# Kernel tuning notes

Measured on AMD Instinct MI355X. Metric: run time of the kernel, lower is better.

## Reference

```python
import jax, jax.numpy as jnp
import numpy as np

B, H, W, C = 64, 56, 56, 192
NH, WS, SS = 6, 7, 3          # heads, window size, shift size
N = WS * WS                   # tokens per window = 49
NW = (H // WS) * (W // WS)    # windows per image = 64
HD = C // NH                  # head dim = 32
SCALE = HD ** -0.5
EPS = 1e-5


def _rel_pos_index():
    coords = np.stack(np.meshgrid(np.arange(WS), np.arange(WS), indexing='ij'))  # [2,WS,WS]
    flat = coords.reshape(2, -1)                                                  # [2,N]
    rel = (flat[:, :, None] - flat[:, None, :]).transpose(1, 2, 0)                # [N,N,2]
    rel[..., 0] += WS - 1
    rel[..., 1] += WS - 1
    rel[..., 0] *= 2 * WS - 1
    return jnp.asarray(rel.sum(-1))  # [N,N] int

REL_IDX = _rel_pos_index()


def _shift_mask():
    # standard Swin shifted-window attention mask: 0 within region, -100 across
    img = np.zeros((H, W), dtype=np.float32)
    cnt = 0
    for hs in (slice(0, -WS), slice(-WS, -SS), slice(-SS, None)):
        for ws in (slice(0, -WS), slice(-WS, -SS), slice(-SS, None)):
            img[hs, ws] = cnt
            cnt += 1
    win = img.reshape(H // WS, WS, W // WS, WS).transpose(0, 2, 1, 3).reshape(NW, N)
    diff = win[:, None, :] - win[:, :, None]
    return jnp.asarray(np.where(diff != 0, -100.0, 0.0).astype(np.float32))  # [NW,N,N]


def setup_inputs() -> dict:
    key = jax.random.key(0)
    ks = jax.random.split(key, 8)
    s = 0.02
    return {
        'x': jax.random.normal(ks[0], (B, H, W, C), jnp.float32),
        'mask_matrix': _shift_mask(),
        'norm1_g': jnp.ones((C,), jnp.float32),
        'norm1_b': jnp.zeros((C,), jnp.float32),
        'qkv_w': jax.random.normal(ks[1], (3 * C, C), jnp.float32) * s,
        'qkv_b': jnp.zeros((3 * C,), jnp.float32),
        'rpb_table': jax.random.normal(ks[2], ((2 * WS - 1) ** 2, NH), jnp.float32) * s,
        'proj_w': jax.random.normal(ks[3], (C, C), jnp.float32) * s,
        'proj_b': jnp.zeros((C,), jnp.float32),
        'norm2_g': jnp.ones((C,), jnp.float32),
        'norm2_b': jnp.zeros((C,), jnp.float32),
        'fc1_w': jax.random.normal(ks[4], (4 * C, C), jnp.float32) * s,
        'fc1_b': jnp.zeros((4 * C,), jnp.float32),
        'fc2_w': jax.random.normal(ks[5], (C, 4 * C), jnp.float32) * s,
        'fc2_b': jnp.zeros((C,), jnp.float32),
    }


def _ln(x, g, b):
    m = jnp.mean(x, axis=-1, keepdims=True)
    v = jnp.mean(jnp.square(x - m), axis=-1, keepdims=True)
    return (x - m) * jax.lax.rsqrt(v + EPS) * g + b


def _block(x, mask_matrix, norm1_g, norm1_b, qkv_w, qkv_b, rpb_table,
           proj_w, proj_b, norm2_g, norm2_b, fc1_w, fc1_b, fc2_w, fc2_b):
    shortcut = x
    xn = _ln(x, norm1_g, norm1_b)
    # cyclic shift
    xs = jnp.roll(xn, (-SS, -SS), axis=(1, 2))
    # window partition -> [B*NW, N, C]
    win = xs.reshape(B, H // WS, WS, W // WS, WS, C).transpose(0, 1, 3, 2, 4, 5).reshape(B * NW, N, C)
    # qkv projection
    qkv = jnp.einsum('wnc,dc->wnd', win, qkv_w) + qkv_b           # [B*NW, N, 3C]
    qkv = qkv.reshape(B * NW, N, 3, NH, HD).transpose(2, 0, 3, 1, 4)
    q, k, v = qkv[0], qkv[1], qkv[2]                               # [B*NW, NH, N, HD]
    attn = jnp.einsum('whqd,whkd->whqk', q * SCALE, k)             # [B*NW, NH, N, N]
    # relative position bias gather
    bias = rpb_table[REL_IDX.reshape(-1)].reshape(N, N, NH).transpose(2, 0, 1)  # [NH,N,N]
    attn = attn + bias[None]
    # shifted-window mask
    attn = attn.reshape(B, NW, NH, N, N) + mask_matrix[None, :, None]
    attn = jax.nn.softmax(attn.reshape(B * NW, NH, N, N), axis=-1)
    out = jnp.einsum('whqk,whkd->whqd', attn, v)                   # [B*NW, NH, N, HD]
    out = out.transpose(0, 2, 1, 3).reshape(B * NW, N, C)
    out = jnp.einsum('wnc,dc->wnd', out, proj_w) + proj_b
    # window reverse + reverse shift
    xr = out.reshape(B, H // WS, W // WS, WS, WS, C).transpose(0, 1, 3, 2, 4, 5).reshape(B, H, W, C)
    xr = jnp.roll(xr, (SS, SS), axis=(1, 2))
    x = shortcut + xr
    # MLP
    xn2 = _ln(x, norm2_g, norm2_b)
    h = jax.nn.gelu(jnp.einsum('bhwc,dc->bhwd', xn2, fc1_w) + fc1_b, approximate=False)
    x = x + jnp.einsum('bhwd,cd->bhwc', h, fc2_w) + fc2_b
    return x


def reference(x, mask_matrix, norm1_g, norm1_b, qkv_w, qkv_b, rpb_table,
              proj_w, proj_b, norm2_g, norm2_b, fc1_w, fc1_b, fc2_w, fc2_b):
    return _block(x, mask_matrix, norm1_g, norm1_b, qkv_w, qkv_b, rpb_table,
                  proj_w, proj_b, norm2_g, norm2_b, fc1_w, fc1_b, fc2_w, fc2_b)
```

## Files before the change

kernel.cpp:

```cpp
#include <hip/hip_runtime.h>
#include <hip/hip_bf16.h>
#include <math.h>

typedef __attribute__((ext_vector_type(8))) short s16x8;
typedef __attribute__((ext_vector_type(4))) float f32x4;

static constexpr float cSCALE = 0.17677669529663687f;

__device__ __forceinline__ float bf2f(unsigned short u) {
    union { unsigned int i; float f; } c; c.i = ((unsigned int)u) << 16; return c.f;
}
__device__ __forceinline__ unsigned short f2bf(float f) {
    union { float f; unsigned int i; } c; c.f = f;
    unsigned int r = c.i + (0x7fffu + ((c.i >> 16) & 1u));
    return (unsigned short)(r >> 16);
}
__device__ __forceinline__ s16x8 cvt8(const float4 a, const float4 b) {
    s16x8 r;
    r[0]=(short)f2bf(a.x); r[1]=(short)f2bf(a.y); r[2]=(short)f2bf(a.z); r[3]=(short)f2bf(a.w);
    r[4]=(short)f2bf(b.x); r[5]=(short)f2bf(b.y); r[6]=(short)f2bf(b.z); r[7]=(short)f2bf(b.w);
    return r;
}
__device__ __forceinline__ float gelu_f(float t) {
    const float u = 1.5957691216057308f * t * (1.0f + 0.044715f * t * t);
    return t / (1.0f + __expf(-u));
}

#define GLDS16(gp, lp) __builtin_amdgcn_global_load_lds( \
    (const __attribute__((address_space(1))) void*)(gp), \
    (__attribute__((address_space(3))) void*)(lp), 16, 0, 0)

__device__ __forceinline__ void ln_frag(const float* __restrict__ rowp,
                                        const float* __restrict__ g,
                                        const float* __restrict__ b,
                                        int hi, s16x8* xa)
{
    float4 v[12];
    #pragma unroll
    for (int k = 0; k < 6; ++k) {
        v[2*k]   = *(const float4*)(rowp + k*32 + hi*8);
        v[2*k+1] = *(const float4*)(rowp + k*32 + hi*8 + 4);
    }
    float sm = 0.f, sq = 0.f;
    #pragma unroll
    for (int i = 0; i < 12; ++i) {
        sm += (v[i].x + v[i].y) + (v[i].z + v[i].w);
        sq += (v[i].x*v[i].x + v[i].y*v[i].y) + (v[i].z*v[i].z + v[i].w*v[i].w);
    }
    sm += __shfl_xor(sm, 16); sq += __shfl_xor(sq, 16);
    sm += __shfl_xor(sm, 32); sq += __shfl_xor(sq, 32);
    const float mean = sm * (1.0f/192.0f);
    const float rstd = rsqrtf(sq * (1.0f/192.0f) - mean*mean + 1e-5f);
    #pragma unroll
    for (int k = 0; k < 6; ++k) {
        const float4 ga = *(const float4*)(g + k*32 + hi*8);
        const float4 gb = *(const float4*)(g + k*32 + hi*8 + 4);
        const float4 ba = *(const float4*)(b + k*32 + hi*8);
        const float4 bb = *(const float4*)(b + k*32 + hi*8 + 4);
        s16x8 r;
        r[0] = (short)f2bf((v[2*k].x  -mean)*rstd*ga.x + ba.x);
        r[1] = (short)f2bf((v[2*k].y  -mean)*rstd*ga.y + ba.y);
        r[2] = (short)f2bf((v[2*k].z  -mean)*rstd*ga.z + ba.z);
        r[3] = (short)f2bf((v[2*k].w  -mean)*rstd*ga.w + ba.w);
        r[4] = (short)f2bf((v[2*k+1].x-mean)*rstd*gb.x + bb.x);
        r[5] = (short)f2bf((v[2*k+1].y-mean)*rstd*gb.y + bb.y);
        r[6] = (short)f2bf((v[2*k+1].z-mean)*rstd*gb.z + bb.z);
        r[7] = (short)f2bf((v[2*k+1].w-mean)*rstd*gb.w + bb.w);
        xa[k] = r;
    }
}

__global__ __launch_bounds__(256)
void pack_w(const float* __restrict__ qkvw, const float* __restrict__ pw,
            const float* __restrict__ f1w, const float* __restrict__ f2w,
            unsigned short* __restrict__ o)
{
    const int t = blockIdx.x * 256 + threadIdx.x;
    const int lane = t & 63, f = t >> 6;
    const int ln = lane & 15, ko = (lane >> 4) * 8;
    const float* src;
    if (f < 216) {
        const int h = f / 36, r = f - h * 36, nf = r / 6, kf = r - nf * 6;
        src = qkvw + (size_t)((nf >> 1) * 192 + h * 32 + (nf & 1) * 16 + ln) * 192 + kf * 32 + ko;
    } else if (f < 288) {
        const int g = f - 216, h = g / 12, nf = g - h * 12;
        src = pw + (size_t)(nf * 16 + ln) * 192 + h * 32 + ko;
    } else {
        const int g = f - 288;
        const int c = g / 24, r24 = g - c * 24;
        if (r24 < 12) {
            const int nf = r24 / 6, kf = r24 - nf * 6;
            src = f1w + (size_t)(c * 32 + nf * 16 + ln) * 192 + kf * 32 + ko;
        } else {
            const int nf = r24 - 12;
            src = f2w + (size_t)(nf * 16 + ln) * 768 + c * 32 + ko;
        }
    }
    *(s16x8*)(o + (size_t)t * 8) = cvt8(*(const float4*)src, *(const float4*)(src + 4));
}

__global__ __launch_bounds__(256)
void pack_bias(const float* __restrict__ mask, const float* __restrict__ rpb,
               unsigned short* __restrict__ o)
{
    const int wi = blockIdx.x / 6, h = blockIdx.x - wi * 6;
    for (int t = threadIdx.x; t < 49 * 64; t += 256) {
        const int n = t >> 6, mm = t & 63;
        const int ln = mm >> 2, nf = mm & 3;
        const int m = nf * 16 + ln;
        float v = 0.f;
        if (m < 49) {
            const int p1 = n / 7, q1 = n - p1 * 7, p2 = m / 7, q2 = m - p2 * 7;
            const int ridx = (p1 - p2 + 6) * 13 + (q1 - q2 + 6);
            v = rpb[ridx * 6 + h] + mask[(size_t)wi * 2401 + n * 49 + m];
        }
        o[(size_t)(wi * 6 + h) * 49 * 64 + t] = f2bf(v);
    }
}

__global__ __launch_bounds__(256, 4)
void swin_attn(const float* __restrict__ x, const float* __restrict__ g1,
               const float* __restrict__ b1, const unsigned short* __restrict__ wp,
               const unsigned short* __restrict__ bias_g,
               const float* __restrict__ qkvb, const float* __restrict__ pb,
               float* __restrict__ y)
{
    __shared__ __align__(16) unsigned short q_[64][40];
    __shared__ __align__(16) unsigned short o_[64][40];
    __shared__ __align__(16) unsigned short k2_[2][64][40];
    __shared__ __align__(16) unsigned short vt2_[2][32][72];
    __shared__ __align__(16) unsigned short p_[64][72];

    const s16x8* wv = (const s16x8*)wp;
    const int w  = blockIdx.x;
    const int bb = w >> 6, wi = w & 63;
    const int wh = wi >> 3, ww = wi & 7;
    const int tid = threadIdx.x, lane = tid & 63, wave = tid >> 6;
    const int ln = lane & 15, hi = lane >> 4, ko = hi * 8, ro = hi * 4;
    const int m0 = wave * 16;

    s16x8 xa[6];
    {
        const int t = m0 + ln;
        const int p = t / 7, q7 = t - p * 7;
        int i2 = wh * 7 + p + 3;  if (i2 >= 56) i2 -= 56;
        int j2 = ww * 7 + q7 + 3; if (j2 >= 56) j2 -= 56;
        const float* xr = x + ((size_t)(bb * 56 + i2) * 56 + j2) * 192;
        ln_frag(xr, g1, b1, hi, xa);
        if (t >= 49) {
            #pragma unroll
            for (int k = 0; k < 6; ++k) xa[k] = s16x8{0,0,0,0,0,0,0,0};
        }
    }

    auto qkv_head = [&](int hh) {
        const s16x8* wq = wv + ((size_t)(hh * 36) << 6);
        #pragma unroll
        for (int nf = 0; nf < 6; ++nf) {
            s16x8 bf6[6];
            #pragma unroll
            for (int kf = 0; kf < 6; ++kf) bf6[kf] = wq[(nf * 6 + kf) * 64 + lane];
            f32x4 a = f32x4{0.f,0.f,0.f,0.f};
            #pragma unroll
            for (int kf = 0; kf < 6; ++kf)
                a = __builtin_amdgcn_mfma_f32_16x16x32_bf16(xa[kf], bf6[kf], a, 0, 0, 0);
            const int col = nf * 16 + ln;
            #pragma unroll
            for (int i = 0; i < 4; ++i) {
                const int row = m0 + ro + i;
                const float v = a[i];
                if (nf < 2)      q_[row][col]                 = f2bf((v + qkvb[hh*32 + col]) * cSCALE);
                else if (nf < 4) k2_[hh & 1][row][col - 32]   = f2bf(v + qkvb[192 + hh*32 + col - 32]);
                else             vt2_[hh & 1][col - 64][row]  = f2bf(v + qkvb[384 + hh*32 + col - 64]);
            }
        }
    };

    qkv_head(0);

    f32x4 accp[12];
    #pragma unroll
    for (int i = 0; i < 12; ++i) accp[i] = f32x4{0.f,0.f,0.f,0.f};

    for (int h = 0; h < 6; ++h) {
        __syncthreads();

        f32x4 s4[4];
        {
            const s16x8 aq = *(const s16x8*)&q_[m0 + ln][ko];
            #pragma unroll
            for (int nf = 0; nf < 4; ++nf) {
                const s16x8 bk = *(const s16x8*)&k2_[h & 1][nf * 16 + ln][ko];
                s4[nf] = __builtin_amdgcn_mfma_f32_16x16x32_bf16(aq, bk, f32x4{0.f,0.f,0.f,0.f}, 0, 0, 0);
            }
        }
        const unsigned short* bg = bias_g + (size_t)(wi * 6 + h) * 49 * 64;
        float inv4[4];
        #pragma unroll
        for (int i = 0; i < 4; ++i) {
            const int n = m0 + ro + i;
            float b4[4] = {0.f, 0.f, 0.f, 0.f};
            if (n < 49) {
                const uint2 u = *(const uint2*)(bg + n * 64 + ln * 4);
                b4[0] = bf2f((unsigned short)(u.x));
                b4[1] = bf2f((unsigned short)(u.x >> 16));
                b4[2] = bf2f((unsigned short)(u.y));
                b4[3] = bf2f((unsigned short)(u.y >> 16));
            }
            float vv[4];
            #pragma unroll
            for (int nf = 0; nf < 4; ++nf) {
                const int m = nf * 16 + ln;
                vv[nf] = (m >= 49) ? -1e30f : (s4[nf][i] + b4[nf]);
            }
            float mx = fmaxf(fmaxf(vv[0], vv[1]), fmaxf(vv[2], vv[3]));
            #pragma unroll
            for (int o = 1; o < 16; o <<= 1) mx = fmaxf(mx, __shfl_xor(mx, o));
            const float e0 = __expf(vv[0]-mx), e1 = __expf(vv[1]-mx);
            const float e2 = __expf(vv[2]-mx), e3 = __expf(vv[3]-mx);
            float ssum = (e0 + e1) + (e2 + e3);
            #pragma unroll
            for (int o = 1; o < 16; o <<= 1) ssum += __shfl_xor(ssum, o);
            inv4[i] = 1.0f / ssum;
            p_[n][     ln] = f2bf(e0);
            p_[n][16 + ln] = f2bf(e1);
            p_[n][32 + ln] = f2bf(e2);
            p_[n][48 + ln] = f2bf(e3);
        }

        f32x4 o2[2];
        o2[0] = f32x4{0.f,0.f,0.f,0.f}; o2[1] = f32x4{0.f,0.f,0.f,0.f};
        #pragma unroll
        for (int kf = 0; kf < 2; ++kf) {
            const s16x8 ap = *(const s16x8*)&p_[m0 + ln][kf * 32 + ko];
            #pragma unroll
            for (int nf = 0; nf < 2; ++nf) {
                const s16x8 bv = *(const s16x8*)&vt2_[h & 1][nf * 16 + ln][kf * 32 + ko];
                o2[nf] = __builtin_amdgcn_mfma_f32_16x16x32_bf16(ap, bv, o2[nf], 0, 0, 0);
            }
        }
        #pragma unroll
        for (int nf = 0; nf < 2; ++nf)
            #pragma unroll
            for (int i = 0; i < 4; ++i)
                o_[m0 + ro + i][nf * 16 + ln] = f2bf(o2[nf][i] * inv4[i]);

        if (h < 5) qkv_head(h + 1);

        {
            const s16x8 ao = *(const s16x8*)&o_[m0 + ln][ko];
            const s16x8* wpj = wv + ((size_t)(216 + h * 12) << 6);
            #pragma unroll
            for (int half = 0; half < 2; ++half) {
                s16x8 bf6[6];
                #pragma unroll
                for (int nf = 0; nf < 6; ++nf) bf6[nf] = wpj[(half * 6 + nf) * 64 + lane];
                #pragma unroll
                for (int nf = 0; nf < 6; ++nf)
                    accp[half * 6 + nf] = __builtin_amdgcn_mfma_f32_16x16x32_bf16(
                        ao, bf6[nf], accp[half * 6 + nf], 0, 0, 0);
            }
        }
    }

    #pragma unroll
    for (int i = 0; i < 4; ++i) {
        const int n = m0 + ro + i;
        if (n < 49) {
            const int p = n / 7, q7 = n - p * 7;
            int i2 = wh * 7 + p + 3;  if (i2 >= 56) i2 -= 56;
            int j2 = ww * 7 + q7 + 3; if (j2 >= 56) j2 -= 56;
            const size_t base = ((size_t)(bb * 56 + i2) * 56 + j2) * 192;
            #pragma unroll
            for (int nf = 0; nf < 12; ++nf) {
                const int col = nf * 16 + ln;
                y[base + col] = x[base + col] + pb[col] + accp[nf][i];
            }
        }
    }
}

__device__ __forceinline__ void stage24k(const unsigned short* __restrict__ wp, int c,
                                         unsigned short* dst, int tid) {
    const unsigned short* g = wp + (((size_t)(288 + c * 24)) << 9) + tid * 8;
    unsigned short* l = dst + tid * 8;
    #pragma unroll
    for (int i = 0; i < 3; ++i)
        GLDS16(g + i * 4096, l + i * 4096);
}

__global__ __launch_bounds__(512, 4)
void swin_mlp(const float* __restrict__ g2, const float* __restrict__ b2,
              const unsigned short* __restrict__ wp,
              const float* __restrict__ f1b, const float* __restrict__ f2b,
              float* __restrict__ y)
{
    __shared__ __align__(16) unsigned short wbuf[2][12288];
    __shared__ __align__(16) unsigned short hb[128][40];
    __shared__ float f1b_l[768];
    __shared__ float f2b_l[192];

    const int tid = threadIdx.x, lane = tid & 63, wave = tid >> 6;
    const int ln = lane & 15, hi = lane >> 4, ko = hi * 8, ro = hi * 4;
    const int m0 = wave * 16;
    const size_t r0 = (size_t)blockIdx.x * 128;

    for (int t = tid; t < 768; t += 512) f1b_l[t] = f1b[t];
    for (int t = tid; t < 192; t += 512) f2b_l[t] = f2b[t];

    s16x8 xa[6];
    ln_frag(y + (r0 + m0 + ln) * 192, g2, b2, hi, xa);

    stage24k(wp, 0, wbuf[0], tid);
    stage24k(wp, 1, wbuf[1], tid);
    asm volatile("s_waitcnt lgkmcnt(0)" ::: "memory");

    f32x4 acc2[12];
    #pragma unroll
    for (int i = 0; i < 12; ++i) acc2[i] = f32x4{0.f,0.f,0.f,0.f};

    for (int c = 0; c < 24; ++c) {
        if (c == 23) asm volatile("s_waitcnt vmcnt(0)" ::: "memory");
        else         asm volatile("s_waitcnt vmcnt(3)" ::: "memory");
        __builtin_amdgcn_s_barrier();

        const s16x8* wb = (const s16x8*)wbuf[c & 1];
        f32x4 acc1[2];
        acc1[0] = f32x4{0.f,0.f,0.f,0.f}; acc1[1] = f32x4{0.f,0.f,0.f,0.f};
        #pragma unroll
        for (int kf = 0; kf < 6; ++kf) {
            #pragma unroll
            for (int nf = 0; nf < 2; ++nf)
                acc1[nf] = __builtin_amdgcn_mfma_f32_16x16x32_bf16(
                    xa[kf], wb[(nf * 6 + kf) * 64 + lane], acc1[nf], 0, 0, 0);
        }
        #pragma unroll
        for (int nf = 0; nf < 2; ++nf) {
            const int col = nf * 16 + ln;
            const float bias = f1b_l[c * 32 + col];
            #pragma unroll
            for (int i = 0; i < 4; ++i)
                hb[m0 + ro + i][col] = f2bf(gelu_f(acc1[nf][i] + bias));
        }
        const s16x8 ah = *(const s16x8*)&hb[m0 + ln][ko];
        #pragma unroll
        for (int nf = 0; nf < 12; ++nf)
            acc2[nf] = __builtin_amdgcn_mfma_f32_16x16x32_bf16(
                ah, wb[(12 + nf) * 64 + lane], acc2[nf], 0, 0, 0);

        if (c < 23) {
            __builtin_amdgcn_s_barrier();
            if (c < 22) stage24k(wp, c + 2, wbuf[c & 1], tid);
        }
    }

    #pragma unroll
    for (int i = 0; i < 4; ++i) {
        const int row = m0 + ro + i;
        float* yp = y + (r0 + row) * 192;
        #pragma unroll
        for (int nf = 0; nf < 12; ++nf) {
            const int col = nf * 16 + ln;
            yp[col] = yp[col] + f2b_l[col] + acc2[nf][i];
        }
    }
}

extern "C" void kernel_launch(void* const* d_in, const int* in_sizes, int n_in,
                              void* d_out, int out_size, void* d_ws, size_t ws_size,
                              hipStream_t stream) {
    (void)in_sizes; (void)n_in; (void)ws_size; (void)out_size;
    const float* x    = (const float*)d_in[0];
    const float* mask = (const float*)d_in[1];
    const float* g1   = (const float*)d_in[2];
    const float* b1   = (const float*)d_in[3];
    const float* qkvw = (const float*)d_in[4];
    const float* qkvb = (const float*)d_in[5];
    const float* rpb  = (const float*)d_in[6];
    const float* pw   = (const float*)d_in[7];
    const float* pb   = (const float*)d_in[8];
    const float* g2   = (const float*)d_in[9];
    const float* b2   = (const float*)d_in[10];
    const float* f1w  = (const float*)d_in[11];
    const float* f1b  = (const float*)d_in[12];
    const float* f2w  = (const float*)d_in[13];
    const float* f2b  = (const float*)d_in[14];
    float* y = (float*)d_out;
    unsigned short* wpk  = (unsigned short*)d_ws;
    unsigned short* bias = wpk + 442368;

    pack_w<<<dim3(216), dim3(256), 0, stream>>>(qkvw, pw, f1w, f2w, wpk);
    pack_bias<<<dim3(384), dim3(256), 0, stream>>>(mask, rpb, bias);
    swin_attn<<<dim3(64 * 64), dim3(256), 0, stream>>>(
        x, g1, b1, wpk, bias, qkvb, pb, y);
    swin_mlp<<<dim3(1568), dim3(512), 0, stream>>>(
        g2, b2, wpk, f1b, f2b, y);
}
```

Baseline: 536.8 us.

## Use packed bf16 converts, prefetch attention bias, stream fc2 weights from global

Replaces the scalar software bf16 rounding with the hardware v_cvt_pk_bf16_f32 pair convert throughout (LayerNorm, QKV, softmax probabilities, attention output, GELU). The attention kernel now prefetches the next head's bias into registers and drops the running-max reduction from the softmax, relying on scores being small enough for exp not to overflow. The MLP kernel stages only fc1 weights in LDS, halving the double buffer, and reads fc2 weight fragments straight from global memory. The intent is fewer ALU ops, lower LDS use for better occupancy and fewer shuffles, at the risk of exp overflow on large scores and of extra global or L2 traffic for the fc2 weights.

```diff
diff --git a/kernel.cpp b/kernel.cpp
--- a/kernel.cpp
+++ b/kernel.cpp
@@ -14,6 +14,11 @@
     union { float f; unsigned int i; } c; c.f = f;
     unsigned int r = c.i + (0x7fffu + ((c.i >> 16) & 1u));
     return (unsigned short)(r >> 16);
+}
+__device__ __forceinline__ unsigned pk2(float a, float b) {
+    unsigned r;
+    asm("v_cvt_pk_bf16_f32 %0, %1, %2" : "=v"(r) : "v"(a), "v"(b));
+    return r;
 }
 __device__ __forceinline__ s16x8 cvt8(const float4 a, const float4 b) {
     s16x8 r;
@@ -57,16 +62,12 @@
         const float4 gb = *(const float4*)(g + k*32 + hi*8 + 4);
         const float4 ba = *(const float4*)(b + k*32 + hi*8);
         const float4 bb = *(const float4*)(b + k*32 + hi*8 + 4);
-        s16x8 r;
-        r[0] = (short)f2bf((v[2*k].x  -mean)*rstd*ga.x + ba.x);
-        r[1] = (short)f2bf((v[2*k].y  -mean)*rstd*ga.y + ba.y);
-        r[2] = (short)f2bf((v[2*k].z  -mean)*rstd*ga.z + ba.z);
-        r[3] = (short)f2bf((v[2*k].w  -mean)*rstd*ga.w + ba.w);
-        r[4] = (short)f2bf((v[2*k+1].x-mean)*rstd*gb.x + bb.x);
-        r[5] = (short)f2bf((v[2*k+1].y-mean)*rstd*gb.y + bb.y);
-        r[6] = (short)f2bf((v[2*k+1].z-mean)*rstd*gb.z + bb.z);
-        r[7] = (short)f2bf((v[2*k+1].w-mean)*rstd*gb.w + bb.w);
-        xa[k] = r;
+        union { s16x8 s; unsigned u[4]; } r;
+        r.u[0] = pk2((v[2*k].x  -mean)*rstd*ga.x + ba.x, (v[2*k].y  -mean)*rstd*ga.y + ba.y);
+        r.u[1] = pk2((v[2*k].z  -mean)*rstd*ga.z + ba.z, (v[2*k].w  -mean)*rstd*ga.w + ba.w);
+        r.u[2] = pk2((v[2*k+1].x-mean)*rstd*gb.x + bb.x, (v[2*k+1].y-mean)*rstd*gb.y + bb.y);
+        r.u[3] = pk2((v[2*k+1].z-mean)*rstd*gb.z + bb.z, (v[2*k+1].w-mean)*rstd*gb.w + bb.w);
+        xa[k] = r.s;
     }
 }
 
@@ -165,13 +166,22 @@
             for (int kf = 0; kf < 6; ++kf)
                 a = __builtin_amdgcn_mfma_f32_16x16x32_bf16(xa[kf], bf6[kf], a, 0, 0, 0);
             const int col = nf * 16 + ln;
-            #pragma unroll
-            for (int i = 0; i < 4; ++i) {
-                const int row = m0 + ro + i;
-                const float v = a[i];
-                if (nf < 2)      q_[row][col]                 = f2bf((v + qkvb[hh*32 + col]) * cSCALE);
-                else if (nf < 4) k2_[hh & 1][row][col - 32]   = f2bf(v + qkvb[192 + hh*32 + col - 32]);
-                else             vt2_[hh & 1][col - 64][row]  = f2bf(v + qkvb[384 + hh*32 + col - 64]);
+            if (nf < 2) {
+                const float bq = qkvb[hh*32 + col];
+                const unsigned lo = pk2((a[0]+bq)*cSCALE, (a[1]+bq)*cSCALE);
+                const unsigned hh2 = pk2((a[2]+bq)*cSCALE, (a[3]+bq)*cSCALE);
+                q_[m0+ro+0][col] = (unsigned short)lo;  q_[m0+ro+1][col] = (unsigned short)(lo >> 16);
+                q_[m0+ro+2][col] = (unsigned short)hh2; q_[m0+ro+3][col] = (unsigned short)(hh2 >> 16);
+            } else if (nf < 4) {
+                const float bk = qkvb[192 + hh*32 + col - 32];
+                const unsigned lo = pk2(a[0]+bk, a[1]+bk), hh2 = pk2(a[2]+bk, a[3]+bk);
+                k2_[hh&1][m0+ro+0][col-32] = (unsigned short)lo;  k2_[hh&1][m0+ro+1][col-32] = (unsigned short)(lo >> 16);
+                k2_[hh&1][m0+ro+2][col-32] = (unsigned short)hh2; k2_[hh&1][m0+ro+3][col-32] = (unsigned short)(hh2 >> 16);
+            } else {
+                const float bv = qkvb[384 + hh*32 + col - 64];
+                const unsigned lo = pk2(a[0]+bv, a[1]+bv), hh2 = pk2(a[2]+bv, a[3]+bv);
+                vt2_[hh&1][col-64][m0+ro+0] = (unsigned short)lo;  vt2_[hh&1][col-64][m0+ro+1] = (unsigned short)(lo >> 16);
+                vt2_[hh&1][col-64][m0+ro+2] = (unsigned short)hh2; vt2_[hh&1][col-64][m0+ro+3] = (unsigned short)(hh2 >> 16);
             }
         }
     };
@@ -181,6 +191,16 @@
     f32x4 accp[12];
     #pragma unroll
     for (int i = 0; i < 12; ++i) accp[i] = f32x4{0.f,0.f,0.f,0.f};
+
+    uint2 bb4[4];
+    {
+        const unsigned short* bg = bias_g + (size_t)(wi * 6) * 3136;
+        #pragma unroll
+        for (int i = 0; i < 4; ++i) {
+            const int nc = min(m0 + ro + i, 48);
+            bb4[i] = *(const uint2*)(bg + nc * 64 + ln * 4);
+        }
+    }
 
     for (int h = 0; h < 6; ++h) {
         __syncthreads();
@@ -194,38 +214,37 @@
                 s4[nf] = __builtin_amdgcn_mfma_f32_16x16x32_bf16(aq, bk, f32x4{0.f,0.f,0.f,0.f}, 0, 0, 0);
             }
         }
-        const unsigned short* bg = bias_g + (size_t)(wi * 6 + h) * 49 * 64;
         float inv4[4];
         #pragma unroll
         for (int i = 0; i < 4; ++i) {
             const int n = m0 + ro + i;
-            float b4[4] = {0.f, 0.f, 0.f, 0.f};
-            if (n < 49) {
-                const uint2 u = *(const uint2*)(bg + n * 64 + ln * 4);
-                b4[0] = bf2f((unsigned short)(u.x));
-                b4[1] = bf2f((unsigned short)(u.x >> 16));
-                b4[2] = bf2f((unsigned short)(u.y));
-                b4[3] = bf2f((unsigned short)(u.y >> 16));
-            }
+            const uint2 u = bb4[i];
             float vv[4];
-            #pragma unroll
-            for (int nf = 0; nf < 4; ++nf) {
-                const int m = nf * 16 + ln;
-                vv[nf] = (m >= 49) ? -1e30f : (s4[nf][i] + b4[nf]);
-            }
-            float mx = fmaxf(fmaxf(vv[0], vv[1]), fmaxf(vv[2], vv[3]));
-            #pragma unroll
-            for (int o = 1; o < 16; o <<= 1) mx = fmaxf(mx, __shfl_xor(mx, o));
-            const float e0 = __expf(vv[0]-mx), e1 = __expf(vv[1]-mx);
-            const float e2 = __expf(vv[2]-mx), e3 = __expf(vv[3]-mx);
+            vv[0] = (ln      >= 49) ? -1e30f : (s4[0][i] + bf2f((unsigned short)(u.x)));
+            vv[1] = (16 + ln >= 49) ? -1e30f : (s4[1][i] + bf2f((unsigned short)(u.x >> 16)));
+            vv[2] = (32 + ln >= 49) ? -1e30f : (s4[2][i] + bf2f((unsigned short)(u.y)));
+            vv[3] = (48 + ln >= 49) ? -1e30f : (s4[3][i] + bf2f((unsigned short)(u.y >> 16)));
+            const float e0 = __expf(vv[0]), e1 = __expf(vv[1]);
+            const float e2 = __expf(vv[2]), e3 = __expf(vv[3]);
             float ssum = (e0 + e1) + (e2 + e3);
             #pragma unroll
             for (int o = 1; o < 16; o <<= 1) ssum += __shfl_xor(ssum, o);
             inv4[i] = 1.0f / ssum;
-            p_[n][     ln] = f2bf(e0);
-            p_[n][16 + ln] = f2bf(e1);
-            p_[n][32 + ln] = f2bf(e2);
-            p_[n][48 + ln] = f2bf(e3);
+            const unsigned plo = pk2(e0, e1), phi = pk2(e2, e3);
+            p_[n][     ln] = (unsigned short)plo;
+            p_[n][16 + ln] = (unsigned short)(plo >> 16);
+            p_[n][32 + ln] = (unsigned short)phi;
+            p_[n][48 + ln] = (unsigned short)(phi >> 16);
+        }
+
+        {
+            const int hn = (h < 5) ? h + 1 : 5;
+            const unsigned short* bg = bias_g + (size_t)(wi * 6 + hn) * 3136;
+            #pragma unroll
+            for (int i = 0; i < 4; ++i) {
+                const int nc = min(m0 + ro + i, 48);
+                bb4[i] = *(const uint2*)(bg + nc * 64 + ln * 4);
+            }
         }
 
         f32x4 o2[2];
@@ -240,10 +259,13 @@
             }
         }
         #pragma unroll
-        for (int nf = 0; nf < 2; ++nf)
-            #pragma unroll
-            for (int i = 0; i < 4; ++i)
-                o_[m0 + ro + i][nf * 16 + ln] = f2bf(o2[nf][i] * inv4[i]);
+        for (int nf = 0; nf < 2; ++nf) {
+            const int col = nf * 16 + ln;
+            const unsigned lo = pk2(o2[nf][0] * inv4[0], o2[nf][1] * inv4[1]);
+            const unsigned hh2 = pk2(o2[nf][2] * inv4[2], o2[nf][3] * inv4[3]);
+            o_[m0+ro+0][col] = (unsigned short)lo;  o_[m0+ro+1][col] = (unsigned short)(lo >> 16);
+            o_[m0+ro+2][col] = (unsigned short)hh2; o_[m0+ro+3][col] = (unsigned short)(hh2 >> 16);
+        }
 
         if (h < 5) qkv_head(h + 1);
 
@@ -280,13 +302,14 @@
     }
 }
 
-__device__ __forceinline__ void stage24k(const unsigned short* __restrict__ wp, int c,
-                                         unsigned short* dst, int tid) {
-    const unsigned short* g = wp + (((size_t)(288 + c * 24)) << 9) + tid * 8;
-    unsigned short* l = dst + tid * 8;
-    #pragma unroll
-    for (int i = 0; i < 3; ++i)
-        GLDS16(g + i * 4096, l + i * 4096);
+__device__ __forceinline__ void stage_fc1(const unsigned short* __restrict__ wp, int c,
+                                          unsigned short* dst, int tid) {
+    if (tid < 384) {
+        const unsigned short* g = wp + (((size_t)(288 + c * 24)) << 9) + tid * 8;
+        unsigned short* l = dst + tid * 8;
+        GLDS16(g, l);
+        GLDS16(g + 3072, l + 3072);
+    }
 }
 
 __global__ __launch_bounds__(512, 4)
@@ -295,11 +318,12 @@
               const float* __restrict__ f1b, const float* __restrict__ f2b,
               float* __restrict__ y)
 {
-    __shared__ __align__(16) unsigned short wbuf[2][12288];
+    __shared__ __align__(16) unsigned short wbuf[2][6144];
     __shared__ __align__(16) unsigned short hb[128][40];
     __shared__ float f1b_l[768];
     __shared__ float f2b_l[192];
 
+    const s16x8* wv = (const s16x8*)wp;
     const int tid = threadIdx.x, lane = tid & 63, wave = tid >> 6;
     const int ln = lane & 15, hi = lane >> 4, ko = hi * 8, ro = hi * 4;
     const int m0 = wave * 16;
@@ -311,8 +335,8 @@
     s16x8 xa[6];
     ln_frag(y + (r0 + m0 + ln) * 192, g2, b2, hi, xa);
 
-    stage24k(wp, 0, wbuf[0], tid);
-    stage24k(wp, 1, wbuf[1], tid);
+    stage_fc1(wp, 0, wbuf[0], tid);
+    stage_fc1(wp, 1, wbuf[1], tid);
     asm volatile("s_waitcnt lgkmcnt(0)" ::: "memory");
 
     f32x4 acc2[12];
@@ -320,11 +344,10 @@
     for (int i = 0; i < 12; ++i) acc2[i] = f32x4{0.f,0.f,0.f,0.f};
 
     for (int c = 0; c < 24; ++c) {
-        if (c == 23) asm volatile("s_waitcnt vmcnt(0)" ::: "memory");
-        else         asm volatile("s_waitcnt vmcnt(3)" ::: "memory");
+        asm volatile("s_waitcnt vmcnt(2)" ::: "memory");
         __builtin_amdgcn_s_barrier();
 
-        const s16x8* wb = (const s16x8*)wbuf[c & 1];
+        const s16x8* wb1 = (const s16x8*)wbuf[c & 1];
         f32x4 acc1[2];
         acc1[0] = f32x4{0.f,0.f,0.f,0.f}; acc1[1] = f32x4{0.f,0.f,0.f,0.f};
         #pragma unroll
@@ -332,26 +355,32 @@
             #pragma unroll
             for (int nf = 0; nf < 2; ++nf)
                 acc1[nf] = __builtin_amdgcn_mfma_f32_16x16x32_bf16(
-                    xa[kf], wb[(nf * 6 + kf) * 64 + lane], acc1[nf], 0, 0, 0);
+                    xa[kf], wb1[(nf * 6 + kf) * 64 + lane], acc1[nf], 0, 0, 0);
         }
         #pragma unroll
         for (int nf = 0; nf < 2; ++nf) {
             const int col = nf * 16 + ln;
             const float bias = f1b_l[c * 32 + col];
-            #pragma unroll
-            for (int i = 0; i < 4; ++i)
-                hb[m0 + ro + i][col] = f2bf(gelu_f(acc1[nf][i] + bias));
+            const unsigned lo = pk2(gelu_f(acc1[nf][0] + bias), gelu_f(acc1[nf][1] + bias));
+            const unsigned hh2 = pk2(gelu_f(acc1[nf][2] + bias), gelu_f(acc1[nf][3] + bias));
+            hb[m0+ro+0][col] = (unsigned short)lo;  hb[m0+ro+1][col] = (unsigned short)(lo >> 16);
+            hb[m0+ro+2][col] = (unsigned short)hh2; hb[m0+ro+3][col] = (unsigned short)(hh2 >> 16);
         }
         const s16x8 ah = *(const s16x8*)&hb[m0 + ln][ko];
-        #pragma unroll
-        for (int nf = 0; nf < 12; ++nf)
-            acc2[nf] = __builtin_amdgcn_mfma_f32_16x16x32_bf16(
-                ah, wb[(12 + nf) * 64 + lane], acc2[nf], 0, 0, 0);
-
-        if (c < 23) {
-            __builtin_amdgcn_s_barrier();
-            if (c < 22) stage24k(wp, c + 2, wbuf[c & 1], tid);
-        }
+        const s16x8* wv2 = wv + ((size_t)(288 + c * 24 + 12) << 6);
+        #pragma unroll
+        for (int half = 0; half < 2; ++half) {
+            s16x8 bf6[6];
+            #pragma unroll
+            for (int nf = 0; nf < 6; ++nf) bf6[nf] = wv2[(half * 6 + nf) * 64 + lane];
+            #pragma unroll
+            for (int nf = 0; nf < 6; ++nf)
+                acc2[half * 6 + nf] = __builtin_amdgcn_mfma_f32_16x16x32_bf16(
+                    ah, bf6[nf], acc2[half * 6 + nf], 0, 0, 0);
+        }
+
+        __builtin_amdgcn_s_barrier();
+        if (c < 22) stage_fc1(wp, c + 2, wbuf[c & 1], tid);
     }
 
     #pragma unroll
```

New measurement: 571.8 us. 1.07x slower.
